# Kernel tuning notes

Hardware: AMD Instinct MI355X
Metric: run time of the kernel (lower is better)

## Reference

```python
import jax, jax.numpy as jnp
import numpy as np

DIM = 768
HEADS = 12
DH = DIM // HEADS
HIDDEN = 4 * DIM
EPS = 1e-5


def layernorm(x, g, b):
    mu = jnp.mean(x, axis=-1, keepdims=True)
    var = jnp.mean(jnp.square(x - mu), axis=-1, keepdims=True)
    return (x - mu) * jax.lax.rsqrt(var + EPS) * g + b


def setup_inputs() -> dict:
    key = jax.random.key(0)
    ks = jax.random.split(key, 12)
    B, N = 8, 1024
    s_in = 1.0 / np.sqrt(DIM)
    s_hid = 1.0 / np.sqrt(HIDDEN)
    return {
        "x": jax.random.normal(ks[0], (B, N, DIM), jnp.float32),
        "q_extra": jax.random.normal(ks[1], (B, N, DIM), jnp.float32),
        "ln1_g": jnp.ones((DIM,), jnp.float32),
        "ln1_b": jnp.zeros((DIM,), jnp.float32),
        "w_kv": jax.random.normal(ks[2], (DIM, 2 * DIM), jnp.float32) * s_in,
        "w_out": jax.random.normal(ks[3], (DIM, DIM), jnp.float32) * s_in,
        "b_out": jnp.zeros((DIM,), jnp.float32),
        "ln2_g": jnp.ones((DIM,), jnp.float32),
        "ln2_b": jnp.zeros((DIM,), jnp.float32),
        "w1": jax.random.normal(ks[4], (DIM, HIDDEN), jnp.float32) * s_in,
        "b1": jnp.zeros((HIDDEN,), jnp.float32),
        "w2": jax.random.normal(ks[5], (HIDDEN, DIM), jnp.float32) * s_hid,
        "b2": jnp.zeros((DIM,), jnp.float32),
    }


def reference(x, q_extra, ln1_g, ln1_b, w_kv, w_out, b_out, ln2_g, ln2_b, w1, b1, w2, b2):
    B, N, C = x.shape
    scale = DH ** (-0.5)

    # pre-norm cross attention
    xn = layernorm(x, ln1_g, ln1_b)
    kv = (xn @ w_kv).reshape(B, N, 2, HEADS, DH)
    k = kv[:, :, 0]  # [B,N,H,Dh]
    v = kv[:, :, 1]
    q = q_extra.reshape(B, N, HEADS, DH)
    dots = jnp.einsum('bnhd,bmhd->bhnm', q, k) * scale
    attn = jax.nn.softmax(dots, axis=-1)
    out = jnp.einsum('bhnm,bmhd->bnhd', attn, v).reshape(B, N, C)
    out = out @ w_out + b_out

    x = x + out  # residual

    # pre-norm MLP
    h = layernorm(x, ln2_g, ln2_b)
    h = jax.nn.gelu(h @ w1 + b1, approximate=False)
    h = h @ w2 + b2
    return x + h
```

## Files before the change

### kernel.cpp

```cpp
#include <hip/hip_runtime.h>

typedef __attribute__((ext_vector_type(8))) short short8;
typedef __attribute__((ext_vector_type(8))) _Float16 half8;
typedef __attribute__((ext_vector_type(2))) __fp16 fp16x2;
typedef __attribute__((ext_vector_type(4))) float float4v;

__device__ __forceinline__ unsigned short f2bf(float f) {
  union { unsigned int i; float f; } x; x.f = f;
  unsigned int r = x.i + 0x7fffu + ((x.i >> 16) & 1u);
  return (unsigned short)(r >> 16);
}

__global__ void ln_kernel(const float* __restrict__ in, const float* __restrict__ g,
                          const float* __restrict__ b, unsigned short* __restrict__ out) {
  const int row = blockIdx.x, t = threadIdx.x;
  const float* xr = in + (size_t)row * 768;
  float v0 = xr[t], v1 = xr[t + 256], v2 = xr[t + 512];
  float s = v0 + v1 + v2;
  float s2 = v0 * v0 + v1 * v1 + v2 * v2;
  for (int off = 32; off > 0; off >>= 1) {
    s += __shfl_xor(s, off, 64);
    s2 += __shfl_xor(s2, off, 64);
  }
  __shared__ float red[8];
  const int wave = t >> 6, lane = t & 63;
  if (lane == 0) { red[wave] = s; red[wave + 4] = s2; }
  __syncthreads();
  s = red[0] + red[1] + red[2] + red[3];
  s2 = red[4] + red[5] + red[6] + red[7];
  const float mu = s * (1.0f / 768.0f);
  const float var = s2 * (1.0f / 768.0f) - mu * mu;
  const float rstd = rsqrtf(var + 1e-5f);
  unsigned short* orow = out + (size_t)row * 768;
  orow[t]       = f2bf((v0 - mu) * rstd * g[t]       + b[t]);
  orow[t + 256] = f2bf((v1 - mu) * rstd * g[t + 256] + b[t + 256]);
  orow[t + 512] = f2bf((v2 - mu) * rstd * g[t + 512] + b[t + 512]);
}

__global__ void wtrans_kernel(const float* __restrict__ in, unsigned short* __restrict__ out,
                              int K, int N) {
  __shared__ float tile[32][33];
  const int k0 = blockIdx.y * 32, n0 = blockIdx.x * 32;
  const int tr = threadIdx.x >> 5, tc = threadIdx.x & 31;
#pragma unroll
  for (int i = 0; i < 4; ++i)
    tile[tr + i * 8][tc] = in[(size_t)(k0 + tr + i * 8) * N + n0 + tc];
  __syncthreads();
#pragma unroll
  for (int i = 0; i < 4; ++i)
    out[(size_t)(n0 + tr + i * 8) * K + k0 + tc] = f2bf(tile[tc][tr + i * 8]);
}

#define SWIZ_BLOCK(GX, TW)                                        \
  const int _id = (int)blockIdx.x;                                \
  const int _gy8 = (int)gridDim.x / (8 * (GX));                   \
  const int _xcd = _id & 7, _jj = _id >> 3;                       \
  const int row0 = (_xcd * _gy8 + _jj / (GX)) * 128;              \
  const int col0 = (_jj % (GX)) * (TW);

__device__ __forceinline__ void gemm128(
    const unsigned short* __restrict__ A, int lda,
    const unsigned short* __restrict__ Bt, int ldb, int K,
    int row0, int col0,
    unsigned short* As, unsigned short* Bs,
    float4v acc[4][4]) {
  const int t = threadIdx.x, lane = t & 63, wave = t >> 6;
  const int quad = lane >> 4, l16 = lane & 15;
  const int wr = wave >> 1, wc = wave & 1;
  const int srow = lane >> 3;
  const int scol = ((lane & 7) ^ srow) * 8;
#pragma unroll
  for (int mt = 0; mt < 4; ++mt)
#pragma unroll
    for (int nt = 0; nt < 4; ++nt) acc[mt][nt] = (float4v)(0.0f);

  for (int kk = 0; kk < K; kk += 64) {
    __syncthreads();
#pragma unroll
    for (int j = 0; j < 4; ++j) {
      const int chunk = wave * 4 + j;
      const int r = chunk * 8 + srow;
      __builtin_amdgcn_global_load_lds(
          (const __attribute__((address_space(1))) unsigned int*)(A + (size_t)(row0 + r) * lda + kk + scol),
          (__attribute__((address_space(3))) unsigned int*)(As + chunk * 512),
          16, 0, 0);
      __builtin_amdgcn_global_load_lds(
          (const __attribute__((address_space(1))) unsigned int*)(Bt + (size_t)(col0 + r) * ldb + kk + scol),
          (__attribute__((address_space(3))) unsigned int*)(Bs + chunk * 512),
          16, 0, 0);
    }
    __syncthreads();
#pragma unroll
    for (int ks = 0; ks < 2; ++ks) {
      const int gsw = ((ks * 4 + quad) ^ (l16 & 7)) * 8;
      short8 af[4], bfv[4];
#pragma unroll
      for (int i = 0; i < 4; ++i) {
        af[i]  = *(const short8*)(As + (wr * 64 + i * 16 + l16) * 64 + gsw);
        bfv[i] = *(const short8*)(Bs + (wc * 64 + i * 16 + l16) * 64 + gsw);
      }
#pragma unroll
      for (int mt = 0; mt < 4; ++mt)
#pragma unroll
        for (int nt = 0; nt < 4; ++nt)
          acc[mt][nt] = __builtin_amdgcn_mfma_f32_16x16x32_bf16(af[mt], bfv[nt], acc[mt][nt], 0, 0, 0);
    }
  }
}

#define GEMM128_PROLOGUE(GX)                                     \
  __shared__ unsigned short As[128 * 64];                        \
  __shared__ unsigned short Bs[128 * 64];                        \
  float4v acc[4][4];                                             \
  SWIZ_BLOCK(GX, 128)                                            \
  const int t = threadIdx.x, lane = t & 63, wave = t >> 6;       \
  const int quad = lane >> 4, l16 = lane & 15;                   \
  const int wr = wave >> 1, wc = wave & 1; (void)t;

__device__ __forceinline__ void gemm12864(
    const unsigned short* __restrict__ A, int lda,
    const unsigned short* __restrict__ Bt, int ldb, int K,
    int row0, int col0,
    unsigned short* As, unsigned short* Bs,
    float4v acc[2][4]) {
  const int t = threadIdx.x, lane = t & 63, wave = t >> 6;
  const int quad = lane >> 4, l16 = lane & 15;
  const int srow = lane >> 3;
  const int scol = ((lane & 7) ^ srow) * 8;
#pragma unroll
  for (int mt = 0; mt < 2; ++mt)
#pragma unroll
    for (int nt = 0; nt < 4; ++nt) acc[mt][nt] = (float4v)(0.0f);

  for (int kk = 0; kk < K; kk += 64) {
    __syncthreads();
#pragma unroll
    for (int j = 0; j < 4; ++j) {
      const int chunk = wave * 4 + j;
      const int r = chunk * 8 + srow;
      __builtin_amdgcn_global_load_lds(
          (const __attribute__((address_space(1))) unsigned int*)(A + (size_t)(row0 + r) * lda + kk + scol),
          (__attribute__((address_space(3))) unsigned int*)(As + chunk * 512),
          16, 0, 0);
    }
#pragma unroll
    for (int j = 0; j < 2; ++j) {
      const int chunk = wave * 2 + j;
      const int r = chunk * 8 + srow;
      __builtin_amdgcn_global_load_lds(
          (const __attribute__((address_space(1))) unsigned int*)(Bt + (size_t)(col0 + r) * ldb + kk + scol),
          (__attribute__((address_space(3))) unsigned int*)(Bs + chunk * 512),
          16, 0, 0);
    }
    __syncthreads();
#pragma unroll
    for (int ks = 0; ks < 2; ++ks) {
      const int gsw = ((ks * 4 + quad) ^ (l16 & 7)) * 8;
      short8 af[2], bfv[4];
#pragma unroll
      for (int i = 0; i < 2; ++i)
        af[i] = *(const short8*)(As + (wave * 32 + i * 16 + l16) * 64 + gsw);
#pragma unroll
      for (int i = 0; i < 4; ++i)
        bfv[i] = *(const short8*)(Bs + (i * 16 + l16) * 64 + gsw);
#pragma unroll
      for (int mt = 0; mt < 2; ++mt)
#pragma unroll
        for (int nt = 0; nt < 4; ++nt)
          acc[mt][nt] = __builtin_amdgcn_mfma_f32_16x16x32_bf16(af[mt], bfv[nt], acc[mt][nt], 0, 0, 0);
    }
  }
}

#define GEMM12864_PROLOGUE(GX)                                   \
  __shared__ unsigned short As[128 * 64];                        \
  __shared__ unsigned short Bs[64 * 64];                         \
  float4v acc[2][4];                                             \
  SWIZ_BLOCK(GX, 64)                                             \
  const int t = threadIdx.x, lane = t & 63, wave = t >> 6;       \
  const int quad = lane >> 4, l16 = lane & 15; (void)t;

__global__ void gemm_kv_kernel(const unsigned short* __restrict__ xn,
                               const unsigned short* __restrict__ wkvt,
                               _Float16* __restrict__ kbuf,
                               _Float16* __restrict__ vtbuf) {
  GEMM128_PROLOGUE(12)
  gemm128(xn, 768, wkvt, 768, 768, row0, col0, As, Bs, acc);
#pragma unroll
  for (int mt = 0; mt < 4; ++mt)
#pragma unroll
    for (int nt = 0; nt < 4; ++nt) {
      const int j = col0 + wc * 64 + nt * 16 + l16;
#pragma unroll
      for (int r = 0; r < 4; ++r) {
        const int m = row0 + wr * 64 + mt * 16 + quad * 4 + r;
        const int bb = m >> 10, n = m & 1023;
        const float c = acc[mt][nt][r];
        if (j < 768) {
          const int hh = j >> 6, d = j & 63;
          kbuf[((size_t)(bb * 12 + hh) * 1024 + n) * 64 + d] = (_Float16)c;
        } else {
          const int j2 = j - 768, hh = j2 >> 6, d = j2 & 63;
          vtbuf[((size_t)(bb * 12 + hh) * 64 + d) * 1024 + n] = (_Float16)c;
        }
      }
    }
}

#define AST 72
#define PST 72
__global__ void attn_kernel(const float* __restrict__ q_extra,
                            const _Float16* __restrict__ kbuf,
                            const _Float16* __restrict__ vtbuf,
                            unsigned short* __restrict__ ao) {
  __shared__ _Float16 Ks[64 * AST];
  __shared__ _Float16 Vs[64 * AST];
  __shared__ _Float16 Ps[4][2][16 * PST];
  const int b = blockIdx.z, h = blockIdx.y, q0 = blockIdx.x * 128;
  const int t = threadIdx.x, lane = t & 63, wave = t >> 6;
  const int quad = lane >> 4, l16 = lane & 15;

  half8 qf[2][2];
#pragma unroll
  for (int qt = 0; qt < 2; ++qt) {
    const float* qp = q_extra +
        ((size_t)((b * 1024 + q0 + qt * 64 + wave * 16 + l16) * 12 + h)) * 64 + quad * 8;
    float4 a0 = *(const float4*)(qp);
    float4 a1 = *(const float4*)(qp + 4);
    float4 c0 = *(const float4*)(qp + 32);
    float4 c1 = *(const float4*)(qp + 36);
    union { fp16x2 h2[4]; half8 h8; } u0, u1;
    u0.h2[0] = __builtin_amdgcn_cvt_pkrtz(a0.x * 0.125f, a0.y * 0.125f);
    u0.h2[1] = __builtin_amdgcn_cvt_pkrtz(a0.z * 0.125f, a0.w * 0.125f);
    u0.h2[2] = __builtin_amdgcn_cvt_pkrtz(a1.x * 0.125f, a1.y * 0.125f);
    u0.h2[3] = __builtin_amdgcn_cvt_pkrtz(a1.z * 0.125f, a1.w * 0.125f);
    u1.h2[0] = __builtin_amdgcn_cvt_pkrtz(c0.x * 0.125f, c0.y * 0.125f);
    u1.h2[1] = __builtin_amdgcn_cvt_pkrtz(c0.z * 0.125f, c0.w * 0.125f);
    u1.h2[2] = __builtin_amdgcn_cvt_pkrtz(c1.x * 0.125f, c1.y * 0.125f);
    u1.h2[3] = __builtin_amdgcn_cvt_pkrtz(c1.z * 0.125f, c1.w * 0.125f);
    qf[qt][0] = u0.h8; qf[qt][1] = u1.h8;
  }

  const _Float16* kb = kbuf + (size_t)(b * 12 + h) * 65536;
  const _Float16* vb = vtbuf + (size_t)(b * 12 + h) * 65536;
  const int srow = t >> 2, su = (t & 3) * 16;

  half8 kp0 = *(const half8*)(kb + (size_t)srow * 64 + su);
  half8 kp1 = *(const half8*)(kb + (size_t)srow * 64 + su + 8);
  half8 vp0 = *(const half8*)(vb + (size_t)srow * 1024 + su);
  half8 vp1 = *(const half8*)(vb + (size_t)srow * 1024 + su + 8);

  float m_s[2] = {-1e30f, -1e30f}, l_s[2] = {0.f, 0.f};
  float4v acc[2][4];
#pragma unroll
  for (int qt = 0; qt < 2; ++qt)
#pragma unroll
    for (int nt = 0; nt < 4; ++nt) acc[qt][nt] = (float4v)(0.f);

  for (int c = 0; c < 16; ++c) {
    __syncthreads();
    *(half8*)(Ks + srow * AST + su)     = kp0;
    *(half8*)(Ks + srow * AST + su + 8) = kp1;
    *(half8*)(Vs + srow * AST + su)     = vp0;
    *(half8*)(Vs + srow * AST + su + 8) = vp1;
    if (c < 15) {
      const int key1 = (c + 1) * 64;
      kp0 = *(const half8*)(kb + (size_t)(key1 + srow) * 64 + su);
      kp1 = *(const half8*)(kb + (size_t)(key1 + srow) * 64 + su + 8);
      vp0 = *(const half8*)(vb + (size_t)srow * 1024 + key1 + su);
      vp1 = *(const half8*)(vb + (size_t)srow * 1024 + key1 + su + 8);
    }
    __syncthreads();

    float4v s[2][4];
#pragma unroll
    for (int kt = 0; kt < 4; ++kt) {
      const _Float16* kr = Ks + (kt * 16 + l16) * AST;
      half8 kf0 = *(const half8*)(kr + quad * 8);
      half8 kf1 = *(const half8*)(kr + 32 + quad * 8);
#pragma unroll
      for (int qt = 0; qt < 2; ++qt) {
        float4v a = (float4v)(0.f);
        a = __builtin_amdgcn_mfma_f32_16x16x32_f16(kf0, qf[qt][0], a, 0, 0, 0);
        a = __builtin_amdgcn_mfma_f32_16x16x32_f16(kf1, qf[qt][1], a, 0, 0, 0);
        s[qt][kt] = a;
      }
    }

    float ab[2][4];
#pragma unroll
    for (int qt = 0; qt < 2; ++qt) {
      float mx = fmaxf(fmaxf(fmaxf(s[qt][0][0], s[qt][0][1]), fmaxf(s[qt][0][2], s[qt][0][3])),
                       fmaxf(fmaxf(s[qt][1][0], s[qt][1][1]), fmaxf(s[qt][1][2], s[qt][1][3])));
      mx = fmaxf(mx, fmaxf(fmaxf(fmaxf(s[qt][2][0], s[qt][2][1]), fmaxf(s[qt][2][2], s[qt][2][3])),
                           fmaxf(fmaxf(s[qt][3][0], s[qt][3][1]), fmaxf(s[qt][3][2], s[qt][3][3]))));
      mx = fmaxf(mx, __shfl_xor(mx, 16, 64));
      mx = fmaxf(mx, __shfl_xor(mx, 32, 64));
      const float mn = fmaxf(m_s[qt], mx);
      const float alpha = __expf(m_s[qt] - mn);
      m_s[qt] = mn;
      _Float16* pw = Ps[wave][qt];
      float sum = 0.0f;
#pragma unroll
      for (int kt = 0; kt < 4; ++kt) {
        const float p0 = __expf(s[qt][kt][0] - mn);
        const float p1 = __expf(s[qt][kt][1] - mn);
        const float p2 = __expf(s[qt][kt][2] - mn);
        const float p3 = __expf(s[qt][kt][3] - mn);
        sum += (p0 + p1) + (p2 + p3);
        union { fp16x2 h2[2]; uint2 u; } pk;
        pk.h2[0] = __builtin_amdgcn_cvt_pkrtz(p0, p1);
        pk.h2[1] = __builtin_amdgcn_cvt_pkrtz(p2, p3);
        *(uint2*)(pw + l16 * PST + kt * 16 + quad * 4) = pk.u;
      }
      sum += __shfl_xor(sum, 16, 64);
      sum += __shfl_xor(sum, 32, 64);
      l_s[qt] = l_s[qt] * alpha + sum;
#pragma unroll
      for (int r = 0; r < 4; ++r) ab[qt][r] = __shfl(alpha, quad * 4 + r, 64);
#pragma unroll
      for (int nt = 0; nt < 4; ++nt)
#pragma unroll
        for (int r = 0; r < 4; ++r) acc[qt][nt][r] *= ab[qt][r];
    }

    half8 pf[2][2];
#pragma unroll
    for (int qt = 0; qt < 2; ++qt) {
      const _Float16* pw = Ps[wave][qt];
      pf[qt][0] = *(const half8*)(pw + l16 * PST + quad * 8);
      pf[qt][1] = *(const half8*)(pw + l16 * PST + 32 + quad * 8);
    }
#pragma unroll
    for (int nt = 0; nt < 4; ++nt) {
      const _Float16* vr = Vs + (nt * 16 + l16) * AST;
      half8 vf0 = *(const half8*)(vr + quad * 8);
      half8 vf1 = *(const half8*)(vr + 32 + quad * 8);
#pragma unroll
      for (int qt = 0; qt < 2; ++qt) {
        acc[qt][nt] = __builtin_amdgcn_mfma_f32_16x16x32_f16(pf[qt][0], vf0, acc[qt][nt], 0, 0, 0);
        acc[qt][nt] = __builtin_amdgcn_mfma_f32_16x16x32_f16(pf[qt][1], vf1, acc[qt][nt], 0, 0, 0);
      }
    }
  }

#pragma unroll
  for (int qt = 0; qt < 2; ++qt) {
    const float inv = 1.0f / l_s[qt];
    float ib[4];
#pragma unroll
    for (int r = 0; r < 4; ++r) ib[r] = __shfl(inv, quad * 4 + r, 64);
#pragma unroll
    for (int nt = 0; nt < 4; ++nt) {
#pragma unroll
      for (int r = 0; r < 4; ++r) {
        const int m = q0 + qt * 64 + wave * 16 + quad * 4 + r;
        ao[(size_t)(b * 1024 + m) * 768 + h * 64 + nt * 16 + l16] =
            f2bf(acc[qt][nt][r] * ib[r]);
      }
    }
  }
}

__global__ void gemm_outproj_kernel(const unsigned short* __restrict__ ao,
                                    const unsigned short* __restrict__ woutt,
                                    const float* __restrict__ b_out,
                                    const float* __restrict__ x,
                                    float* __restrict__ x2) {
  GEMM12864_PROLOGUE(12)
  gemm12864(ao, 768, woutt, 768, 768, row0, col0, As, Bs, acc);
#pragma unroll
  for (int mt = 0; mt < 2; ++mt)
#pragma unroll
    for (int nt = 0; nt < 4; ++nt) {
      const int j = col0 + nt * 16 + l16;
#pragma unroll
      for (int r = 0; r < 4; ++r) {
        const int m = row0 + wave * 32 + mt * 16 + quad * 4 + r;
        const size_t idx = (size_t)m * 768 + j;
        x2[idx] = acc[mt][nt][r] + b_out[j] + x[idx];
      }
    }
}

__global__ void gemm_mlp1_kernel(const unsigned short* __restrict__ h,
                                 const unsigned short* __restrict__ w1t,
                                 const float* __restrict__ b1,
                                 unsigned short* __restrict__ h1) {
  GEMM128_PROLOGUE(24)
  gemm128(h, 768, w1t, 768, 768, row0, col0, As, Bs, acc);
#pragma unroll
  for (int mt = 0; mt < 4; ++mt)
#pragma unroll
    for (int nt = 0; nt < 4; ++nt) {
      const int j = col0 + wc * 64 + nt * 16 + l16;
#pragma unroll
      for (int r = 0; r < 4; ++r) {
        const int m = row0 + wr * 64 + mt * 16 + quad * 4 + r;
        const float y = acc[mt][nt][r] + b1[j];
        const float ge = 0.5f * y * (1.0f + erff(y * 0.70710678118654752f));
        h1[(size_t)m * 3072 + j] = f2bf(ge);
      }
    }
}

__global__ void gemm_mlp2_kernel(const unsigned short* __restrict__ h1,
                                 const unsigned short* __restrict__ w2t,
                                 const float* __restrict__ b2,
                                 const float* __restrict__ x2,
                                 float* __restrict__ out) {
  GEMM12864_PROLOGUE(12)
  gemm12864(h1, 3072, w2t, 3072, 3072, row0, col0, As, Bs, acc);
#pragma unroll
  for (int mt = 0; mt < 2; ++mt)
#pragma unroll
    for (int nt = 0; nt < 4; ++nt) {
      const int j = col0 + nt * 16 + l16;
#pragma unroll
      for (int r = 0; r < 4; ++r) {
        const int m = row0 + wave * 32 + mt * 16 + quad * 4 + r;
        const size_t idx = (size_t)m * 768 + j;
        out[idx] = acc[mt][nt][r] + b2[j] + x2[idx];
      }
    }
}

extern "C" void kernel_launch(void* const* d_in, const int* in_sizes, int n_in,
                              void* d_out, int out_size, void* d_ws, size_t ws_size,
                              hipStream_t stream) {
  const float* x       = (const float*)d_in[0];
  const float* q_extra = (const float*)d_in[1];
  const float* ln1_g   = (const float*)d_in[2];
  const float* ln1_b   = (const float*)d_in[3];
  const float* w_kv    = (const float*)d_in[4];
  const float* w_out   = (const float*)d_in[5];
  const float* b_out   = (const float*)d_in[6];
  const float* ln2_g   = (const float*)d_in[7];
  const float* ln2_b   = (const float*)d_in[8];
  const float* w1      = (const float*)d_in[9];
  const float* b1      = (const float*)d_in[10];
  const float* w2      = (const float*)d_in[11];
  const float* b2      = (const float*)d_in[12];
  float* out = (float*)d_out;

  char* ws = (char*)d_ws;
  unsigned short* xn    = (unsigned short*)(ws);
  _Float16*       kbuf  = (_Float16*)(ws + 12582912);
  _Float16*       vtbuf = (_Float16*)(ws + 25165824);
  unsigned short* ao    = (unsigned short*)(ws + 37748736);
  float*          x2    = (float*)(ws + 50331648);
  unsigned short* h1    = (unsigned short*)(ws + 75497472);
  unsigned short* hbuf  = xn;
  unsigned short* wkvt  = ao;
  unsigned short* woutt = h1;
  unsigned short* w1t   = (unsigned short*)kbuf;
  unsigned short* w2t   = (unsigned short*)vtbuf;

  ln_kernel<<<8192, 256, 0, stream>>>(x, ln1_g, ln1_b, xn);
  wtrans_kernel<<<dim3(48, 24), 256, 0, stream>>>(w_kv, wkvt, 768, 1536);
  wtrans_kernel<<<dim3(24, 24), 256, 0, stream>>>(w_out, woutt, 768, 768);
  gemm_kv_kernel<<<768, 256, 0, stream>>>(xn, wkvt, kbuf, vtbuf);
  attn_kernel<<<dim3(8, 12, 8), 256, 0, stream>>>(q_extra, kbuf, vtbuf, ao);
  wtrans_kernel<<<dim3(96, 24), 256, 0, stream>>>(w1, w1t, 768, 3072);
  wtrans_kernel<<<dim3(24, 96), 256, 0, stream>>>(w2, w2t, 3072, 768);
  gemm_outproj_kernel<<<768, 256, 0, stream>>>(ao, woutt, b_out, x, x2);
  ln_kernel<<<8192, 256, 0, stream>>>(x2, ln2_g, ln2_b, hbuf);
  gemm_mlp1_kernel<<<1536, 256, 0, stream>>>(hbuf, w1t, b1, h1);
  gemm_mlp2_kernel<<<768, 256, 0, stream>>>(h1, w2t, b2, x2, out);
}
```

Before: 389.7 us.

## Halve attention query tile, remap grid for K/V L2 reuse, use exp2

```diff
diff --git a/kernel.cpp b/kernel.cpp
--- a/kernel.cpp
+++ b/kernel.cpp
@@ -1,4 +1,5 @@
 #include <hip/hip_runtime.h>
+#include <math.h>
 
 typedef __attribute__((ext_vector_type(8))) short short8;
 typedef __attribute__((ext_vector_type(8))) _Float16 half8;
@@ -215,30 +216,33 @@
                             unsigned short* __restrict__ ao) {
   __shared__ _Float16 Ks[64 * AST];
   __shared__ _Float16 Vs[64 * AST];
-  __shared__ _Float16 Ps[4][2][16 * PST];
-  const int b = blockIdx.z, h = blockIdx.y, q0 = blockIdx.x * 128;
+  __shared__ _Float16 Ps[4][16 * PST];
+  const int id = (int)blockIdx.x;
+  const int pair = id % 96, qb = id / 96;
+  const int h = pair >> 3, b = pair & 7;
+  const int q0 = qb * 64;
   const int t = threadIdx.x, lane = t & 63, wave = t >> 6;
   const int quad = lane >> 4, l16 = lane & 15;
 
-  half8 qf[2][2];
-#pragma unroll
-  for (int qt = 0; qt < 2; ++qt) {
+  const float QS = 0.125f * 1.44269504088896f;
+  half8 qf0, qf1;
+  {
     const float* qp = q_extra +
-        ((size_t)((b * 1024 + q0 + qt * 64 + wave * 16 + l16) * 12 + h)) * 64 + quad * 8;
+        ((size_t)((b * 1024 + q0 + wave * 16 + l16) * 12 + h)) * 64 + quad * 8;
     float4 a0 = *(const float4*)(qp);
     float4 a1 = *(const float4*)(qp + 4);
     float4 c0 = *(const float4*)(qp + 32);
     float4 c1 = *(const float4*)(qp + 36);
     union { fp16x2 h2[4]; half8 h8; } u0, u1;
-    u0.h2[0] = __builtin_amdgcn_cvt_pkrtz(a0.x * 0.125f, a0.y * 0.125f);
-    u0.h2[1] = __builtin_amdgcn_cvt_pkrtz(a0.z * 0.125f, a0.w * 0.125f);
-    u0.h2[2] = __builtin_amdgcn_cvt_pkrtz(a1.x * 0.125f, a1.y * 0.125f);
-    u0.h2[3] = __builtin_amdgcn_cvt_pkrtz(a1.z * 0.125f, a1.w * 0.125f);
-    u1.h2[0] = __builtin_amdgcn_cvt_pkrtz(c0.x * 0.125f, c0.y * 0.125f);
-    u1.h2[1] = __builtin_amdgcn_cvt_pkrtz(c0.z * 0.125f, c0.w * 0.125f);
-    u1.h2[2] = __builtin_amdgcn_cvt_pkrtz(c1.x * 0.125f, c1.y * 0.125f);
-    u1.h2[3] = __builtin_amdgcn_cvt_pkrtz(c1.z * 0.125f, c1.w * 0.125f);
-    qf[qt][0] = u0.h8; qf[qt][1] = u1.h8;
+    u0.h2[0] = __builtin_amdgcn_cvt_pkrtz(a0.x * QS, a0.y * QS);
+    u0.h2[1] = __builtin_amdgcn_cvt_pkrtz(a0.z * QS, a0.w * QS);
+    u0.h2[2] = __builtin_amdgcn_cvt_pkrtz(a1.x * QS, a1.y * QS);
+    u0.h2[3] = __builtin_amdgcn_cvt_pkrtz(a1.z * QS, a1.w * QS);
+    u1.h2[0] = __builtin_amdgcn_cvt_pkrtz(c0.x * QS, c0.y * QS);
+    u1.h2[1] = __builtin_amdgcn_cvt_pkrtz(c0.z * QS, c0.w * QS);
+    u1.h2[2] = __builtin_amdgcn_cvt_pkrtz(c1.x * QS, c1.y * QS);
+    u1.h2[3] = __builtin_amdgcn_cvt_pkrtz(c1.z * QS, c1.w * QS);
+    qf0 = u0.h8; qf1 = u1.h8;
   }
 
   const _Float16* kb = kbuf + (size_t)(b * 12 + h) * 65536;
@@ -250,12 +254,11 @@
   half8 vp0 = *(const half8*)(vb + (size_t)srow * 1024 + su);
   half8 vp1 = *(const half8*)(vb + (size_t)srow * 1024 + su + 8);
 
-  float m_s[2] = {-1e30f, -1e30f}, l_s[2] = {0.f, 0.f};
-  float4v acc[2][4];
-#pragma unroll
-  for (int qt = 0; qt < 2; ++qt)
-#pragma unroll
-    for (int nt = 0; nt < 4; ++nt) acc[qt][nt] = (float4v)(0.f);
+  float m_s = -1e30f, l_s = 0.0f;
+  float4v acc[4];
+  acc[0] = (float4v)(0.f); acc[1] = (float4v)(0.f);
+  acc[2] = (float4v)(0.f); acc[3] = (float4v)(0.f);
+  _Float16* pw = Ps[wave];
 
   for (int c = 0; c < 16; ++c) {
     __syncthreads();
@@ -272,92 +275,76 @@
     }
     __syncthreads();
 
-    float4v s[2][4];
+    float4v s[4];
 #pragma unroll
     for (int kt = 0; kt < 4; ++kt) {
       const _Float16* kr = Ks + (kt * 16 + l16) * AST;
       half8 kf0 = *(const half8*)(kr + quad * 8);
       half8 kf1 = *(const half8*)(kr + 32 + quad * 8);
-#pragma unroll
-      for (int qt = 0; qt < 2; ++qt) {
-        float4v a = (float4v)(0.f);
-        a = __builtin_amdgcn_mfma_f32_16x16x32_f16(kf0, qf[qt][0], a, 0, 0, 0);
-        a = __builtin_amdgcn_mfma_f32_16x16x32_f16(kf1, qf[qt][1], a, 0, 0, 0);
-        s[qt][kt] = a;
-      }
-    }
-
-    float ab[2][4];
-#pragma unroll
-    for (int qt = 0; qt < 2; ++qt) {
-      float mx = fmaxf(fmaxf(fmaxf(s[qt][0][0], s[qt][0][1]), fmaxf(s[qt][0][2], s[qt][0][3])),
-                       fmaxf(fmaxf(s[qt][1][0], s[qt][1][1]), fmaxf(s[qt][1][2], s[qt][1][3])));
-      mx = fmaxf(mx, fmaxf(fmaxf(fmaxf(s[qt][2][0], s[qt][2][1]), fmaxf(s[qt][2][2], s[qt][2][3])),
-                           fmaxf(fmaxf(s[qt][3][0], s[qt][3][1]), fmaxf(s[qt][3][2], s[qt][3][3]))));
-      mx = fmaxf(mx, __shfl_xor(mx, 16, 64));
-      mx = fmaxf(mx, __shfl_xor(mx, 32, 64));
-      const float mn = fmaxf(m_s[qt], mx);
-      const float alpha = __expf(m_s[qt] - mn);
-      m_s[qt] = mn;
-      _Float16* pw = Ps[wave][qt];
-      float sum = 0.0f;
-#pragma unroll
-      for (int kt = 0; kt < 4; ++kt) {
-        const float p0 = __expf(s[qt][kt][0] - mn);
-        const float p1 = __expf(s[qt][kt][1] - mn);
-        const float p2 = __expf(s[qt][kt][2] - mn);
-        const float p3 = __expf(s[qt][kt][3] - mn);
-        sum += (p0 + p1) + (p2 + p3);
-        union { fp16x2 h2[2]; uint2 u; } pk;
-        pk.h2[0] = __builtin_amdgcn_cvt_pkrtz(p0, p1);
-        pk.h2[1] = __builtin_amdgcn_cvt_pkrtz(p2, p3);
-        *(uint2*)(pw + l16 * PST + kt * 16 + quad * 4) = pk.u;
-      }
-      sum += __shfl_xor(sum, 16, 64);
-      sum += __shfl_xor(sum, 32, 64);
-      l_s[qt] = l_s[qt] * alpha + sum;
-#pragma unroll
-      for (int r = 0; r < 4; ++r) ab[qt][r] = __shfl(alpha, quad * 4 + r, 64);
-#pragma unroll
-      for (int nt = 0; nt < 4; ++nt)
-#pragma unroll
-        for (int r = 0; r < 4; ++r) acc[qt][nt][r] *= ab[qt][r];
-    }
-
-    half8 pf[2][2];
-#pragma unroll
-    for (int qt = 0; qt < 2; ++qt) {
-      const _Float16* pw = Ps[wave][qt];
-      pf[qt][0] = *(const half8*)(pw + l16 * PST + quad * 8);
-      pf[qt][1] = *(const half8*)(pw + l16 * PST + 32 + quad * 8);
-    }
+      float4v a = (float4v)(0.f);
+      a = __builtin_amdgcn_mfma_f32_16x16x32_f16(kf0, qf0, a, 0, 0, 0);
+      a = __builtin_amdgcn_mfma_f32_16x16x32_f16(kf1, qf1, a, 0, 0, 0);
+      s[kt] = a;
+    }
+
+    float mx = fmaxf(fmaxf(fmaxf(s[0][0], s[0][1]), fmaxf(s[0][2], s[0][3])),
+                     fmaxf(fmaxf(s[1][0], s[1][1]), fmaxf(s[1][2], s[1][3])));
+    mx = fmaxf(mx, fmaxf(fmaxf(fmaxf(s[2][0], s[2][1]), fmaxf(s[2][2], s[2][3])),
+                         fmaxf(fmaxf(s[3][0], s[3][1]), fmaxf(s[3][2], s[3][3]))));
+    mx = fmaxf(mx, __shfl_xor(mx, 16, 64));
+    mx = fmaxf(mx, __shfl_xor(mx, 32, 64));
+    const float mn = fmaxf(m_s, mx);
+    const float alpha = exp2f(m_s - mn);
+    m_s = mn;
+
+    float sum = 0.0f;
+#pragma unroll
+    for (int kt = 0; kt < 4; ++kt) {
+      const float p0 = exp2f(s[kt][0] - mn);
+      const float p1 = exp2f(s[kt][1] - mn);
+      const float p2 = exp2f(s[kt][2] - mn);
+      const float p3 = exp2f(s[kt][3] - mn);
+      sum += (p0 + p1) + (p2 + p3);
+      union { fp16x2 h2[2]; uint2 u; } pk;
+      pk.h2[0] = __builtin_amdgcn_cvt_pkrtz(p0, p1);
+      pk.h2[1] = __builtin_amdgcn_cvt_pkrtz(p2, p3);
+      *(uint2*)(pw + l16 * PST + kt * 16 + quad * 4) = pk.u;
+    }
+    sum += __shfl_xor(sum, 16, 64);
+    sum += __shfl_xor(sum, 32, 64);
+    l_s = l_s * alpha + sum;
+
+    float ab[4];
+#pragma unroll
+    for (int r = 0; r < 4; ++r) ab[r] = __shfl(alpha, quad * 4 + r, 64);
+#pragma unroll
+    for (int nt = 0; nt < 4; ++nt)
+#pragma unroll
+      for (int r = 0; r < 4; ++r) acc[nt][r] *= ab[r];
+
+    half8 pf0 = *(const half8*)(pw + l16 * PST + quad * 8);
+    half8 pf1 = *(const half8*)(pw + l16 * PST + 32 + quad * 8);
 #pragma unroll
     for (int nt = 0; nt < 4; ++nt) {
       const _Float16* vr = Vs + (nt * 16 + l16) * AST;
       half8 vf0 = *(const half8*)(vr + quad * 8);
       half8 vf1 = *(const half8*)(vr + 32 + quad * 8);
-#pragma unroll
-      for (int qt = 0; qt < 2; ++qt) {
-        acc[qt][nt] = __builtin_amdgcn_mfma_f32_16x16x32_f16(pf[qt][0], vf0, acc[qt][nt], 0, 0, 0);
-        acc[qt][nt] = __builtin_amdgcn_mfma_f32_16x16x32_f16(pf[qt][1], vf1, acc[qt][nt], 0, 0, 0);
-      }
-    }
-  }
-
-#pragma unroll
-  for (int qt = 0; qt < 2; ++qt) {
-    const float inv = 1.0f / l_s[qt];
-    float ib[4];
-#pragma unroll
-    for (int r = 0; r < 4; ++r) ib[r] = __shfl(inv, quad * 4 + r, 64);
-#pragma unroll
-    for (int nt = 0; nt < 4; ++nt) {
-#pragma unroll
-      for (int r = 0; r < 4; ++r) {
-        const int m = q0 + qt * 64 + wave * 16 + quad * 4 + r;
-        ao[(size_t)(b * 1024 + m) * 768 + h * 64 + nt * 16 + l16] =
-            f2bf(acc[qt][nt][r] * ib[r]);
-      }
+      acc[nt] = __builtin_amdgcn_mfma_f32_16x16x32_f16(pf0, vf0, acc[nt], 0, 0, 0);
+      acc[nt] = __builtin_amdgcn_mfma_f32_16x16x32_f16(pf1, vf1, acc[nt], 0, 0, 0);
+    }
+  }
+
+  const float inv = 1.0f / l_s;
+  float ib[4];
+#pragma unroll
+  for (int r = 0; r < 4; ++r) ib[r] = __shfl(inv, quad * 4 + r, 64);
+#pragma unroll
+  for (int nt = 0; nt < 4; ++nt) {
+#pragma unroll
+    for (int r = 0; r < 4; ++r) {
+      const int m = q0 + wave * 16 + quad * 4 + r;
+      ao[(size_t)(b * 1024 + m) * 768 + h * 64 + nt * 16 + l16] =
+          f2bf(acc[nt][r] * ib[r]);
     }
   }
 }
@@ -460,7 +447,7 @@
   wtrans_kernel<<<dim3(48, 24), 256, 0, stream>>>(w_kv, wkvt, 768, 1536);
   wtrans_kernel<<<dim3(24, 24), 256, 0, stream>>>(w_out, woutt, 768, 768);
   gemm_kv_kernel<<<768, 256, 0, stream>>>(xn, wkvt, kbuf, vtbuf);
-  attn_kernel<<<dim3(8, 12, 8), 256, 0, stream>>>(q_extra, kbuf, vtbuf, ao);
+  attn_kernel<<<1536, 256, 0, stream>>>(q_extra, kbuf, vtbuf, ao);
   wtrans_kernel<<<dim3(96, 24), 256, 0, stream>>>(w1, w1t, 768, 3072);
   wtrans_kernel<<<dim3(24, 96), 256, 0, stream>>>(w2, w2t, 3072, 768);
   gemm_outproj_kernel<<<768, 256, 0, stream>>>(ao, woutt, b_out, x, x2);
```

Result: faster. 378.2 us (-2.9%).
